# Performance work log

Measured on AMD Instinct MI355X. Metric: run time of the kernel, lower is better.

Reference implementation:

```python
import jax, jax.numpy as jnp
import numpy as np

THR = 0.05
BETA = 0.9181805491303656
SLOPE = 13.42287274232855

# straight-through estimator: heaviside fwd, identity bwd
@jax.custom_vjp
def spike_ste(x):
    return (x > 0).astype(x.dtype)
def _ste_fwd(x):
    return (x > 0).astype(x.dtype), None
def _ste_bwd(res, g):
    return (g,)
spike_ste.defvjp(_ste_fwd, _ste_bwd)

# fast sigmoid surrogate: heaviside fwd, grad 1/(slope*|x|+1)^2 bwd
@jax.custom_vjp
def spike_fs(x):
    return (x > 0).astype(x.dtype)
def _fs_fwd(x):
    return (x > 0).astype(x.dtype), x
def _fs_bwd(x, g):
    return (g / (SLOPE * jnp.abs(x) + 1.0) ** 2,)
spike_fs.defvjp(_fs_fwd, _fs_bwd)

def _conv(x, w, b):
    y = jax.lax.conv_general_dilated(x, w, (1, 1), 'SAME', dimension_numbers=('NCHW', 'OIHW', 'NCHW'))
    return y + b[None, :, None, None]

def _maxpool2(x):
    return jax.lax.reduce_window(x, -jnp.inf, jax.lax.max, (1, 1, 2, 2), (1, 1, 2, 2), 'VALID')

def _sconvlstm(x, syn, mem, w, b):
    # snntorch SConvLSTM: conv over cat(input, hidden) -> 4 gates; reset_mechanism='none'
    gates = _conv(jnp.concatenate([x, mem], axis=1), w, b)
    cc_i, cc_f, cc_g, cc_o = jnp.split(gates, 4, axis=1)
    syn = jax.nn.sigmoid(cc_f) * syn + jax.nn.sigmoid(cc_i) * jnp.tanh(cc_g)
    mem = jax.nn.sigmoid(cc_o) * jnp.tanh(syn)
    spk = spike_ste(_maxpool2(mem) - THR)  # spike on max-pooled membrane
    return spk, syn, mem

def _leaky(cur, mem):
    # snntorch Leaky, reset_mechanism='subtract'; reset computed from previous mem, detached
    reset = jax.lax.stop_gradient((mem > THR).astype(mem.dtype))
    mem = BETA * mem + cur - reset * THR
    spk = spike_fs(mem - THR)
    return spk, mem

def setup_inputs():
    key = jax.random.key(0)
    ks = jax.random.split(key, 11)
    T, B, H, W = 25, 64, 16, 128
    x = jax.random.normal(ks[0], (T, B, H, W), jnp.float32)
    def cw(k, o, i):
        return jax.random.normal(k, (o, i, 3, 3), jnp.float32) / np.float32(np.sqrt(i * 9))
    w1 = cw(ks[1], 64, 17)
    b1 = jax.random.normal(ks[2], (64,), jnp.float32) * 0.01
    w2 = cw(ks[3], 128, 48)
    b2 = jax.random.normal(ks[4], (128,), jnp.float32) * 0.01
    w3 = cw(ks[5], 256, 96)
    b3 = jax.random.normal(ks[6], (256,), jnp.float32) * 0.01
    fc1_w = jax.random.normal(ks[7], (512, 2048), jnp.float32) / np.float32(np.sqrt(2048))
    fc1_b = jax.random.normal(ks[8], (512,), jnp.float32) * 0.01
    fc2_w = jax.random.normal(ks[9], (2, 512), jnp.float32) / np.float32(np.sqrt(512))
    fc2_b = jax.random.normal(ks[10], (2,), jnp.float32) * 0.01
    return dict(x=x, w1=w1, b1=b1, w2=w2, b2=b2, w3=w3, b3=b3,
                fc1_w=fc1_w, fc1_b=fc1_b, fc2_w=fc2_w, fc2_b=fc2_b)

def reference(x, w1, b1, w2, b2, w3, b3, fc1_w, fc1_b, fc2_w, fc2_b):
    T, B, H, W = x.shape
    z = lambda c, h, w: jnp.zeros((B, c, h, w), x.dtype)
    carry = (z(16, H, W), z(16, H, W),
             z(32, H // 2, W // 2), z(32, H // 2, W // 2),
             z(64, H // 4, W // 4), z(64, H // 4, W // 4),
             jnp.zeros((B, 512), x.dtype), jnp.zeros((B, 2), x.dtype))
    def step(carry, xt):
        syn1, mem1, syn2, mem2, syn3, mem3, mem4, mem5 = carry
        spk1, syn1, mem1 = _sconvlstm(xt[:, None], syn1, mem1, w1, b1)
        spk2, syn2, mem2 = _sconvlstm(spk1, syn2, mem2, w2, b2)
        spk3, syn3, mem3 = _sconvlstm(spk2, syn3, mem3, w3, b3)
        cur4 = spk3.reshape(B, -1) @ fc1_w.T + fc1_b  # dropout = identity (eval mode)
        spk4, mem4 = _leaky(cur4, mem4)
        cur5 = spk4 @ fc2_w.T + fc2_b
        spk5, mem5 = _leaky(cur5, mem5)
        return (syn1, mem1, syn2, mem2, syn3, mem3, mem4, mem5), (spk5, mem5)
    _, (spk_rec, mem_rec) = jax.lax.scan(step, carry, x)
    return spk_rec, mem_rec
```

## Files before the change

### kernel.cpp

```cpp
#include <hip/hip_runtime.h>
#include <math.h>
#include <stdint.h>

#define THR  0.05f
#define BETA 0.9181805491303656f
#define B_SZ 64
#define T_STEPS 25

using h8    = __attribute__((ext_vector_type(8))) _Float16;
using f32x4 = __attribute__((ext_vector_type(4))) float;

__device__ __forceinline__ float sigf(float x) { return 1.0f / (1.0f + __expf(-x)); }
__device__ __forceinline__ float tanh_fast(float x) {
    const float xc = fminf(fmaxf(x, -10.0f), 10.0f);
    const float e = __expf(2.0f * xc);
    return (e - 1.0f) / (e + 1.0f);
}

__global__ __launch_bounds__(256) void repack_kernel(
    const float* __restrict__ wt, float* __restrict__ wr, int Ch, int CIN)
{
    const int n = 4 * Ch * CIN * 9;
    for (int i = blockIdx.x * 256 + threadIdx.x; i < n; i += gridDim.x * 256) {
        const int g   = i & 3;
        const int tap = (i >> 2) % 9;
        const int ci  = (i / 36) % CIN;
        const int c   = i / (36 * CIN);
        wr[i] = wt[(((size_t)(g * Ch + c)) * CIN + ci) * 9 + tap];
    }
}

__global__ __launch_bounds__(256) void repack_mfma_kernel(
    const float* __restrict__ wt, _Float16* __restrict__ whi, _Float16* __restrict__ wlo,
    int Ch, int CIN, int KS)
{
    const int NG = (4 * Ch) / 16;
    const int n = 9 * KS * NG * 512;
    for (int i = blockIdx.x * 256 + threadIdx.x; i < n; i += gridDim.x * 256) {
        const int j   = i & 7;
        const int l   = (i >> 3) & 63;
        const int ng  = (i >> 9) % NG;
        const int ks  = (i / (512 * NG)) % KS;
        const int tap = i / (512 * NG * KS);
        const int o   = ng * 16 + (l & 15);
        const int ci  = ks * 32 + ((l >> 4) << 3) + j;
        const float w = (ci < CIN) ? wt[((size_t)o * CIN + ci) * 9 + tap] : 0.0f;
        const _Float16 hi = (_Float16)w;
        whi[i] = hi;
        wlo[i] = (_Float16)(w - (float)hi);
    }
}

template<int CSPK, int Ch, int H, int W, int H_T, int KS, int CIN_S, bool POOL>
__global__ __launch_bounds__(256) void convlstm_mfma(
    const float* __restrict__ xin,
    const float* __restrict__ memin,
    const float* __restrict__ synin,
    float* __restrict__ synout,
    float* __restrict__ memout,
    const _Float16* __restrict__ whi,
    const _Float16* __restrict__ wlo,
    const float* __restrict__ bias)
{
    constexpr int CIN   = CSPK + Ch;
    constexpr int W2    = W + 2;
    constexpr int ROWS  = (H_T + 2) * W2;
    constexpr int NELEM = ROWS * CIN_S + 16;
    constexpr int NCG   = Ch / 16;
    constexpr int MSPLIT = H / H_T;
    constexpr int M_T   = H_T * W;
    constexpr int WM    = M_T / 4;
    constexpr int MF    = WM / 16;
    constexpr int NG    = (4 * Ch) / 16;
    constexpr int SPAIRS = W / 2;
    constexpr int NCP   = CIN / 2;
    static_assert(WM % 16 == 0 && W % 16 == 0, "");
    static_assert(KS * 32 <= CIN_S + 16, "last k-read must stay inside NELEM slack");
    static_assert(CIN_S >= CIN, "channels must fit the padded stride");
    static_assert(CIN % 2 == 0 && CSPK % 2 == 0 && CIN_S % 2 == 0, "pair packing");

    __shared__ _Float16 tileH[NELEM];
    __shared__ _Float16 tileL[NELEM];

    const int tid = threadIdx.x;
    const int bid = blockIdx.x;
    const int cg = bid % NCG;
    const int ms = (bid / NCG) % MSPLIT;
    const int b  = bid / (NCG * MSPLIT);
    const int y0 = ms * H_T;
    const int c0 = cg * 16;

    {
        uint32_t* p0 = (uint32_t*)tileH;
        uint32_t* p1 = (uint32_t*)tileL;
        for (int i = tid; i < NELEM / 2; i += 256) { p0[i] = 0u; p1[i] = 0u; }
    }
    __syncthreads();

    for (int i = tid; i < NCP * (H_T + 2) * SPAIRS; i += 256) {
        const int px = i % SPAIRS;
        const int ry = (i / SPAIRS) % (H_T + 2);
        const int cp = i / (SPAIRS * (H_T + 2));
        const int ci = 2 * cp;
        const int y  = y0 + ry - 1;
        if (y < 0 || y >= H) continue;
        const int x0 = 2 * px;
        float v[2][2];
        #pragma unroll
        for (int d = 0; d < 2; ++d) {
            const int c = ci + d;
            if (POOL && c < CSPK) {
                const float* mp = xin + (((size_t)b * CSPK + c) * (2 * H) + 2 * y) * (2 * W) + 2 * x0;
                const float4 q0 = *(const float4*)mp;
                const float4 q1 = *(const float4*)(mp + 2 * W);
                v[d][0] = ((fmaxf(fmaxf(q0.x, q0.y), fmaxf(q1.x, q1.y)) - THR) > 0.0f) ? 1.0f : 0.0f;
                v[d][1] = ((fmaxf(fmaxf(q0.z, q0.w), fmaxf(q1.z, q1.w)) - THR) > 0.0f) ? 1.0f : 0.0f;
            } else if (c < CSPK) {
                const float2 q = *(const float2*)(xin + (((size_t)b * CSPK + c) * H + y) * W + x0);
                v[d][0] = q.x; v[d][1] = q.y;
            } else {
                const float2 q = *(const float2*)(memin + (((size_t)b * Ch + (c - CSPK)) * H + y) * W + x0);
                v[d][0] = q.x; v[d][1] = q.y;
            }
        }
        #pragma unroll
        for (int dx = 0; dx < 2; ++dx) {
            const int off = (ry * W2 + x0 + dx + 1) * CIN_S + ci;
            const _Float16 h0 = (_Float16)v[0][dx];
            const _Float16 h1 = (_Float16)v[1][dx];
            const _Float16 l0 = (_Float16)(v[0][dx] - (float)h0);
            const _Float16 l1 = (_Float16)(v[1][dx] - (float)h1);
            const uint32_t ph = (uint32_t)__builtin_bit_cast(uint16_t, h0)
                              | ((uint32_t)__builtin_bit_cast(uint16_t, h1) << 16);
            const uint32_t pl = (uint32_t)__builtin_bit_cast(uint16_t, l0)
                              | ((uint32_t)__builtin_bit_cast(uint16_t, l1) << 16);
            *(uint32_t*)(tileH + off) = ph;
            *(uint32_t*)(tileL + off) = pl;
        }
    }
    __syncthreads();

    const int lane = tid & 63;
    const int wid  = tid >> 6;
    const int l15  = lane & 15;
    const int lk8  = (lane >> 4) << 3;

    f32x4 acc[MF][4];
    #pragma unroll
    for (int g = 0; g < 4; ++g) {
        const float bb = bias[g * Ch + c0 + l15];
        #pragma unroll
        for (int m = 0; m < MF; ++m) acc[m][g] = f32x4{bb, bb, bb, bb};
    }

    #pragma unroll 3
    for (int tap = 0; tap < 9; ++tap) {
        const int dy = tap / 3, dx = tap % 3;
        #pragma unroll
        for (int ks = 0; ks < KS; ++ks) {
            h8 bh[4], bl[4];
            #pragma unroll
            for (int g = 0; g < 4; ++g) {
                const size_t base = ((((size_t)tap * KS + ks) * NG + g * NCG + cg) * 64 + lane) * 8;
                bh[g] = *(const h8*)(whi + base);
                bl[g] = *(const h8*)(wlo + base);
            }
            #pragma unroll
            for (int m = 0; m < MF; ++m) {
                const int pxf = wid * WM + m * 16;
                const int yl = pxf / W;
                const int xf = pxf % W;
                const int off = ((yl + dy) * W2 + xf + l15 + dx) * CIN_S + ks * 32 + lk8;
                const h8 ah = *(const h8*)(tileH + off);
                const h8 al = *(const h8*)(tileL + off);
                #pragma unroll
                for (int g = 0; g < 4; ++g) {
                    acc[m][g] = __builtin_amdgcn_mfma_f32_16x16x32_f16(ah, bh[g], acc[m][g], 0, 0, 0);
                    acc[m][g] = __builtin_amdgcn_mfma_f32_16x16x32_f16(ah, bl[g], acc[m][g], 0, 0, 0);
                    acc[m][g] = __builtin_amdgcn_mfma_f32_16x16x32_f16(al, bh[g], acc[m][g], 0, 0, 0);
                }
            }
        }
    }

    #pragma unroll
    for (int m = 0; m < MF; ++m) {
        const int pxf = wid * WM + m * 16;
        const int yl = pxf / W;
        const int xf = pxf % W;
        const int c = c0 + l15;
        #pragma unroll
        for (int j = 0; j < 4; ++j) {
            const int x = xf + ((lane >> 4) << 2) + j;
            const size_t gaddr = (((size_t)b * Ch + c) * H + (y0 + yl)) * W + x;
            const float gi = acc[m][0][j], gf = acc[m][1][j];
            const float gg = acc[m][2][j], go = acc[m][3][j];
            const float syn = sigf(gf) * synin[gaddr] + sigf(gi) * tanh_fast(gg);
            synout[gaddr] = syn;
            memout[gaddr] = sigf(go) * tanh_fast(syn);
        }
    }
}

template<int Cin, int Ch, int H, int W, int R, int CSPLIT, int CHUNK,
         bool POOL_IN, int MINW, int P, int NT>
__global__ __launch_bounds__(NT, MINW) void conv_lstm(
    const float* __restrict__ xin,
    const float* __restrict__ memin,
    const float* __restrict__ synin,
    float* __restrict__ synout,
    float* __restrict__ memout,
    const float* __restrict__ wr,
    const float* __restrict__ bias)
{
    constexpr int CIN = Cin + Ch;
    constexpr int R2 = R + 2;
    constexpr int SW = W + 4;
    constexpr int ROWLANES = W / P;
    constexpr int SQ = W / 4;
    constexpr int NROUNDS = CIN / CHUNK;
    constexpr int NW = NT / 64;
    constexpr int CITERS = Ch / (CSPLIT * NW);
    static_assert(R * ROWLANES == 64, "");
    static_assert(CIN % CHUNK == 0, "");
    static_assert(W % 4 == 0, "");

    __shared__ float tile[CHUNK * R2 * SW];

    const int tid = threadIdx.x;
    const int bid = blockIdx.x;
    const int cs = bid % CSPLIT;
    const int rs = (bid / CSPLIT) % (H / R);
    const int b  = bid / (CSPLIT * (H / R));
    const int r0 = rs * R;
    const int c0 = cs * (Ch / CSPLIT);

    const int lane = tid & 63;
    const int wid  = tid >> 6;
    const int ly   = lane / ROWLANES;
    const int lx   = P * (lane % ROWLANES);
    const int gy_out = r0 + ly;

    int cu[CITERS];
    #pragma unroll
    for (int k = 0; k < CITERS; ++k)
        cu[k] = __builtin_amdgcn_readfirstlane(c0 + k * NW + wid);

    float acc[CITERS][4 * P];
    #pragma unroll
    for (int k = 0; k < CITERS; ++k) {
        const float bi = bias[cu[k]];
        const float bf = bias[cu[k] + Ch];
        const float bg = bias[cu[k] + 2 * Ch];
        const float bo = bias[cu[k] + 3 * Ch];
        #pragma unroll
        for (int p = 0; p < P; ++p) {
            acc[k][0 * P + p] = bi;
            acc[k][1 * P + p] = bf;
            acc[k][2 * P + p] = bg;
            acc[k][3 * P + p] = bo;
        }
    }

    for (int rd = 0; rd < NROUNDS; ++rd) {
        const int k0 = rd * CHUNK;
        if (rd) __syncthreads();

        for (int i = tid; i < CHUNK * R2 * 4; i += NT) {
            const int col = i & 3;
            const int row = i >> 2;
            tile[row * SW + (col == 0 ? 0 : W + col)] = 0.0f;
        }
        for (int i = tid; i < CHUNK * R2 * SQ; i += NT) {
            const int q   = i % SQ;
            const int ry  = (i / SQ) % R2;
            const int cil = i / (SQ * R2);
            const int ci  = k0 + cil;
            const int gy  = r0 + ry - 1;
            float v0 = 0.0f, v1 = 0.0f, v2 = 0.0f, v3 = 0.0f;
            if (gy >= 0 && gy < H) {
                if (POOL_IN && ci < Cin) {
                    const float* mp = xin + (((size_t)b * Cin + ci) * (2 * H) + 2 * gy) * (2 * W) + 8 * q;
                    const float4 a0 = *(const float4*)mp;
                    const float4 a1 = *(const float4*)(mp + 4);
                    const float4 b0 = *(const float4*)(mp + 2 * W);
                    const float4 b1 = *(const float4*)(mp + 2 * W + 4);
                    v0 = ((fmaxf(fmaxf(a0.x, a0.y), fmaxf(b0.x, b0.y)) - THR) > 0.0f) ? 1.0f : 0.0f;
                    v1 = ((fmaxf(fmaxf(a0.z, a0.w), fmaxf(b0.z, b0.w)) - THR) > 0.0f) ? 1.0f : 0.0f;
                    v2 = ((fmaxf(fmaxf(a1.x, a1.y), fmaxf(b1.x, b1.y)) - THR) > 0.0f) ? 1.0f : 0.0f;
                    v3 = ((fmaxf(fmaxf(a1.z, a1.w), fmaxf(b1.z, b1.w)) - THR) > 0.0f) ? 1.0f : 0.0f;
                } else if (ci < Cin) {
                    const float4 a = *(const float4*)(xin + (((size_t)b * Cin + ci) * H + gy) * W + 4 * q);
                    v0 = a.x; v1 = a.y; v2 = a.z; v3 = a.w;
                } else {
                    const float4 a = *(const float4*)(memin + (((size_t)b * Ch + (ci - Cin)) * H + gy) * W + 4 * q);
                    v0 = a.x; v1 = a.y; v2 = a.z; v3 = a.w;
                }
            }
            const int t0 = (cil * R2 + ry) * SW + 1 + 4 * q;
            tile[t0]     = v0;
            tile[t0 + 1] = v1;
            tile[t0 + 2] = v2;
            tile[t0 + 3] = v3;
        }
        __syncthreads();

        #pragma unroll 1
        for (int cil = 0; cil < CHUNK; ++cil) {
            float s[3][P + 2];
            #pragma unroll
            for (int dy = 0; dy < 3; ++dy) {
                const float* rp = &tile[(cil * R2 + ly + dy) * SW + lx];
                if constexpr (P == 4) {
                    const float4 a  = *(const float4*)rp;
                    const float2 e  = *(const float2*)(rp + 4);
                    s[dy][0] = a.x; s[dy][1] = a.y; s[dy][2] = a.z; s[dy][3] = a.w;
                    s[dy][4] = e.x; s[dy][5] = e.y;
                } else {
                    const float2 a  = *(const float2*)rp;
                    const float2 e  = *(const float2*)(rp + 2);
                    s[dy][0] = a.x; s[dy][1] = a.y; s[dy][2] = e.x; s[dy][3] = e.y;
                }
            }
            #pragma unroll
            for (int k = 0; k < CITERS; ++k) {
                const float* wp = wr + ((size_t)cu[k] * CIN + (k0 + cil)) * 36;
                #pragma unroll
                for (int tap = 0; tap < 9; ++tap) {
                    const int dy = tap / 3, dx = tap % 3;
                    const float wi  = wp[tap * 4 + 0];
                    const float wf  = wp[tap * 4 + 1];
                    const float wg_ = wp[tap * 4 + 2];
                    const float wo  = wp[tap * 4 + 3];
                    #pragma unroll
                    for (int p = 0; p < P; ++p) {
                        const float v = s[dy][p + dx];
                        acc[k][0 * P + p] = fmaf(v, wi,  acc[k][0 * P + p]);
                        acc[k][1 * P + p] = fmaf(v, wf,  acc[k][1 * P + p]);
                        acc[k][2 * P + p] = fmaf(v, wg_, acc[k][2 * P + p]);
                        acc[k][3 * P + p] = fmaf(v, wo,  acc[k][3 * P + p]);
                    }
                }
            }
        }
    }

    #pragma unroll
    for (int k = 0; k < CITERS; ++k) {
        const int c = c0 + k * NW + wid;
        const size_t base = (((size_t)b * Ch + c) * H + gy_out) * W + lx;
        float sv[P], so[P], mo[P];
        if constexpr (P == 4) {
            const float4 q = *(const float4*)(synin + base);
            sv[0] = q.x; sv[1] = q.y; sv[2] = q.z; sv[3] = q.w;
        } else {
            const float2 q = *(const float2*)(synin + base);
            sv[0] = q.x; sv[1] = q.y;
        }
        #pragma unroll
        for (int p = 0; p < P; ++p) {
            const float syn = sigf(acc[k][1 * P + p]) * sv[p]
                            + sigf(acc[k][0 * P + p]) * tanh_fast(acc[k][2 * P + p]);
            so[p] = syn;
            mo[p] = sigf(acc[k][3 * P + p]) * tanh_fast(syn);
        }
        if constexpr (P == 4) {
            *(float4*)(synout + base) = make_float4(so[0], so[1], so[2], so[3]);
            *(float4*)(memout + base) = make_float4(mo[0], mo[1], mo[2], mo[3]);
        } else {
            *(float2*)(synout + base) = make_float2(so[0], so[1]);
            *(float2*)(memout + base) = make_float2(mo[0], mo[1]);
        }
    }
}

__global__ __launch_bounds__(256) void fc1_pool_kernel(
    const float* __restrict__ m3,
    const float* __restrict__ wt,
    const float* __restrict__ bias,
    float* __restrict__ mem4,
    float* __restrict__ spk4)
{
    const int wid = (blockIdx.x * 256 + threadIdx.x) >> 6;
    const int lane = threadIdx.x & 63;
    const int og = wid & 63;
    const int b = wid >> 6;
    const int o0 = og * 8;

    float acc[8] = {0, 0, 0, 0, 0, 0, 0, 0};
    for (int it = 0; it < 8; ++it) {
        const int k = (it * 64 + lane) * 4;
        const int c = k >> 5;
        const int rem = k & 31;
        const int ph = rem >> 4;
        const int pw = rem & 15;
        const float* mp = m3 + (((size_t)b * 64 + c) * 4 + 2 * ph) * 32 + 2 * pw;
        const float4 r0 = *(const float4*)mp;
        const float4 r1 = *(const float4*)(mp + 4);
        const float4 q0 = *(const float4*)(mp + 32);
        const float4 q1 = *(const float4*)(mp + 36);
        float4 sv;
        sv.x = ((fmaxf(fmaxf(r0.x, r0.y), fmaxf(q0.x, q0.y)) - THR) > 0.0f) ? 1.0f : 0.0f;
        sv.y = ((fmaxf(fmaxf(r0.z, r0.w), fmaxf(q0.z, q0.w)) - THR) > 0.0f) ? 1.0f : 0.0f;
        sv.z = ((fmaxf(fmaxf(r1.x, r1.y), fmaxf(q1.x, q1.y)) - THR) > 0.0f) ? 1.0f : 0.0f;
        sv.w = ((fmaxf(fmaxf(r1.z, r1.w), fmaxf(q1.z, q1.w)) - THR) > 0.0f) ? 1.0f : 0.0f;
        #pragma unroll
        for (int j = 0; j < 8; ++j) {
            const float4 wv = *(const float4*)(wt + (size_t)(o0 + j) * 2048 + k);
            acc[j] = fmaf(sv.x, wv.x, acc[j]);
            acc[j] = fmaf(sv.y, wv.y, acc[j]);
            acc[j] = fmaf(sv.z, wv.z, acc[j]);
            acc[j] = fmaf(sv.w, wv.w, acc[j]);
        }
    }
    float mine = 0.0f;
    #pragma unroll
    for (int j = 0; j < 8; ++j) {
        float a = acc[j];
        #pragma unroll
        for (int off = 32; off; off >>= 1) a += __shfl_xor(a, off, 64);
        if (lane == j) mine = a;
    }
    if (lane < 8) {
        const int o = o0 + lane;
        const float cur = mine + bias[o];
        const int i4 = b * 512 + o;
        float m = mem4[i4];
        const float reset = (m > THR) ? 1.0f : 0.0f;
        m = BETA * m + cur - reset * THR;
        spk4[i4] = ((m - THR) > 0.0f) ? 1.0f : 0.0f;
        mem4[i4] = m;
    }
}

__global__ __launch_bounds__(256) void fc2_kernel(
    const float* __restrict__ spk4,
    const float* __restrict__ wt,
    const float* __restrict__ bias,
    float* __restrict__ mem5,
    float* __restrict__ out_spk,
    float* __restrict__ out_mem)
{
    const int wid = (blockIdx.x * 256 + threadIdx.x) >> 6;
    const int lane = threadIdx.x & 63;
    if (wid >= 2 * B_SZ) return;
    const int o = wid & 1;
    const int b = wid >> 1;
    const float* wr = wt + (size_t)o * 512;
    const float* sr = spk4 + (size_t)b * 512;
    float acc = 0.0f;
    #pragma unroll
    for (int i = 0; i < 8; ++i)
        acc = fmaf(sr[lane + i * 64], wr[lane + i * 64], acc);
    #pragma unroll
    for (int off = 32; off; off >>= 1) acc += __shfl_down(acc, off, 64);
    if (lane == 0) {
        const float cur = acc + bias[o];
        const int i5 = b * 2 + o;
        float m = mem5[i5];
        const float reset = (m > THR) ? 1.0f : 0.0f;
        m = BETA * m + cur - reset * THR;
        out_spk[i5] = ((m - THR) > 0.0f) ? 1.0f : 0.0f;
        out_mem[i5] = m;
        mem5[i5] = m;
    }
}

extern "C" void kernel_launch(void* const* d_in, const int* in_sizes, int n_in,
                              void* d_out, int out_size, void* d_ws, size_t ws_size,
                              hipStream_t stream) {
    (void)in_sizes; (void)n_in; (void)out_size; (void)ws_size;

    const float* x    = (const float*)d_in[0];
    const float* w1   = (const float*)d_in[1];
    const float* b1   = (const float*)d_in[2];
    const float* w2   = (const float*)d_in[3];
    const float* b2   = (const float*)d_in[4];
    const float* w3   = (const float*)d_in[5];
    const float* b3   = (const float*)d_in[6];
    const float* fc1w = (const float*)d_in[7];
    const float* fc1b = (const float*)d_in[8];
    const float* fc2w = (const float*)d_in[9];
    const float* fc2b = (const float*)d_in[10];

    float* out = (float*)d_out;
    float* ws = (float*)d_ws;

    const size_t N1 = (size_t)B_SZ * 16 * 16 * 128;
    const size_t N2 = (size_t)B_SZ * 32 * 8 * 64;
    const size_t N3 = (size_t)B_SZ * 64 * 4 * 32;

    size_t off = 0;
    float* syn1  = ws + off; off += N1;
    float* mem1a = ws + off; off += N1;
    float* syn2  = ws + off; off += N2;
    float* mem2a = ws + off; off += N2;
    float* syn3  = ws + off; off += N3;
    float* mem3a = ws + off; off += N3;
    float* mem4  = ws + off; off += (size_t)B_SZ * 512;
    float* mem5  = ws + off; off += (size_t)B_SZ * 2;
    const size_t zero_elems = off;
    float* mem1b = ws + off; off += N1;
    float* mem2b = ws + off; off += N2;
    float* mem3b = ws + off; off += N3;
    float* spk4  = ws + off; off += (size_t)B_SZ * 512;
    float* wr1   = ws + off; off += (size_t)4 * 16 * 17 * 9;
    _Float16* whi2 = (_Float16*)(ws + off); off += 36864;
    _Float16* wlo2 = (_Float16*)(ws + off); off += 36864;
    _Float16* whi3 = (_Float16*)(ws + off); off += 110592;
    _Float16* wlo3 = (_Float16*)(ws + off); off += 110592;

    (void)hipMemsetAsync(d_ws, 0, zero_elems * sizeof(float), stream);

    repack_kernel<<<64, 256, 0, stream>>>(w1, wr1, 16, 17);
    repack_mfma_kernel<<<288, 256, 0, stream>>>(w2, whi2, wlo2, 32, 48, 2);
    repack_mfma_kernel<<<864, 256, 0, stream>>>(w3, whi3, wlo3, 64, 96, 3);

    float* m1r = mem1a; float* m1w = mem1b;
    float* m2r = mem2a; float* m2w = mem2b;
    float* m3r = mem3a; float* m3w = mem3b;

    for (int t = 0; t < T_STEPS; ++t) {
        const float* xt = x + (size_t)t * B_SZ * 16 * 128;

        conv_lstm<1, 16, 16, 128, 2, 1, 17, false, 4, 4, 512><<<512, 512, 0, stream>>>(
            xt, m1r, syn1, syn1, m1w, wr1, b1);

        convlstm_mfma<16, 32, 8, 64, 2, 2, 56, true><<<512, 256, 0, stream>>>(
            m1w, m2r, syn2, syn2, m2w, whi2, wlo2, b2);

        convlstm_mfma<32, 64, 4, 32, 2, 3, 104, true><<<512, 256, 0, stream>>>(
            m2w, m3r, syn3, syn3, m3w, whi3, wlo3, b3);

        fc1_pool_kernel<<<1024, 256, 0, stream>>>(m3w, fc1w, fc1b, mem4, spk4);
        fc2_kernel<<<32, 256, 0, stream>>>(
            spk4, fc2w, fc2b, mem5, out + (size_t)t * 2 * B_SZ,
            out + 3200 + (size_t)t * 2 * B_SZ);

        float* tmp;
        tmp = m1r; m1r = m1w; m1w = tmp;
        tmp = m2r; m2r = m2w; m2w = tmp;
        tmp = m3r; m3r = m3w; m3w = tmp;
    }
}
```

Baseline: 2.781 ms.

## Fold previous-step fc2 into layer-1 conv launch and retune layer-2 grid split

The separate per-step fc2 launch is removed. The previous timestep's fc2 plus Leaky update now runs in one extra block appended to the layer-1 ConvLSTM launch, and a final fc2 launch after the loop handles the last step. This cuts one kernel launch per timestep and overlaps the small fc2 work with the conv. Separately, the layer-2 MFMA conv template parameter changes from 2 to 1 and its grid doubles to 1024 blocks, which likely means finer row tiling for more parallelism.

```diff
diff --git a/kernel.cpp b/kernel.cpp
--- a/kernel.cpp
+++ b/kernel.cpp
@@ -211,7 +211,14 @@
     float* __restrict__ synout,
     float* __restrict__ memout,
     const float* __restrict__ wr,
-    const float* __restrict__ bias)
+    const float* __restrict__ bias,
+    const float* __restrict__ spk4_prev,
+    const float* __restrict__ fc2w,
+    const float* __restrict__ fc2b,
+    float* __restrict__ mem5,
+    float* __restrict__ out_spk,
+    float* __restrict__ out_mem,
+    int fc2_on)
 {
     constexpr int CIN = Cin + Ch;
     constexpr int R2 = R + 2;
@@ -221,6 +228,8 @@
     constexpr int NROUNDS = CIN / CHUNK;
     constexpr int NW = NT / 64;
     constexpr int CITERS = Ch / (CSPLIT * NW);
+    constexpr int NBLK = 0;
+    (void)NBLK;
     static_assert(R * ROWLANES == 64, "");
     static_assert(CIN % CHUNK == 0, "");
     static_assert(W % 4 == 0, "");
@@ -229,14 +238,43 @@
 
     const int tid = threadIdx.x;
     const int bid = blockIdx.x;
+    const int lane = tid & 63;
+    const int wid  = tid >> 6;
+
+    if (bid >= CSPLIT * (H / R) * B_SZ) {
+        if (fc2_on) {
+            for (int task = wid; task < 2 * B_SZ; task += NW) {
+                const int o = task & 1;
+                const int b2 = task >> 1;
+                const float* wrow = fc2w + (size_t)o * 512;
+                const float* sr = spk4_prev + (size_t)b2 * 512;
+                float acc2 = 0.0f;
+                #pragma unroll
+                for (int i = 0; i < 8; ++i)
+                    acc2 = fmaf(sr[lane + i * 64], wrow[lane + i * 64], acc2);
+                #pragma unroll
+                for (int off = 32; off; off >>= 1) acc2 += __shfl_down(acc2, off, 64);
+                if (lane == 0) {
+                    const float cur = acc2 + fc2b[o];
+                    const int i5 = b2 * 2 + o;
+                    float m = mem5[i5];
+                    const float reset = (m > THR) ? 1.0f : 0.0f;
+                    m = BETA * m + cur - reset * THR;
+                    out_spk[i5] = ((m - THR) > 0.0f) ? 1.0f : 0.0f;
+                    out_mem[i5] = m;
+                    mem5[i5] = m;
+                }
+            }
+        }
+        return;
+    }
+
     const int cs = bid % CSPLIT;
     const int rs = (bid / CSPLIT) % (H / R);
     const int b  = bid / (CSPLIT * (H / R));
     const int r0 = rs * R;
     const int c0 = cs * (Ch / CSPLIT);
 
-    const int lane = tid & 63;
-    const int wid  = tid >> 6;
     const int ly   = lane / ROWLANES;
     const int lx   = P * (lane % ROWLANES);
     const int gy_out = r0 + ly;
@@ -522,24 +560,27 @@
 
     for (int t = 0; t < T_STEPS; ++t) {
         const float* xt = x + (size_t)t * B_SZ * 16 * 128;
-
-        conv_lstm<1, 16, 16, 128, 2, 1, 17, false, 4, 4, 512><<<512, 512, 0, stream>>>(
-            xt, m1r, syn1, syn1, m1w, wr1, b1);
-
-        convlstm_mfma<16, 32, 8, 64, 2, 2, 56, true><<<512, 256, 0, stream>>>(
+        const size_t oprev = (t > 0) ? (size_t)(t - 1) * 2 * B_SZ : 0;
+
+        conv_lstm<1, 16, 16, 128, 2, 1, 17, false, 4, 4, 512><<<513, 512, 0, stream>>>(
+            xt, m1r, syn1, syn1, m1w, wr1, b1,
+            spk4, fc2w, fc2b, mem5, out + oprev, out + 3200 + oprev, t > 0 ? 1 : 0);
+
+        convlstm_mfma<16, 32, 8, 64, 1, 2, 56, true><<<1024, 256, 0, stream>>>(
             m1w, m2r, syn2, syn2, m2w, whi2, wlo2, b2);
 
         convlstm_mfma<32, 64, 4, 32, 2, 3, 104, true><<<512, 256, 0, stream>>>(
             m2w, m3r, syn3, syn3, m3w, whi3, wlo3, b3);
 
         fc1_pool_kernel<<<1024, 256, 0, stream>>>(m3w, fc1w, fc1b, mem4, spk4);
-        fc2_kernel<<<32, 256, 0, stream>>>(
-            spk4, fc2w, fc2b, mem5, out + (size_t)t * 2 * B_SZ,
-            out + 3200 + (size_t)t * 2 * B_SZ);
 
         float* tmp;
         tmp = m1r; m1r = m1w; m1w = tmp;
         tmp = m2r; m2r = m2w; m2w = tmp;
         tmp = m3r; m3r = m3w; m3w = tmp;
     }
-}
+
+    const size_t olast = (size_t)(T_STEPS - 1) * 2 * B_SZ;
+    fc2_kernel<<<32, 256, 0, stream>>>(
+        spk4, fc2w, fc2b, mem5, out + olast, out + 3200 + olast);
+}
```

After: 3.206 ms. 15.3% more time.
